# Kernel optimization log

Measured on AMD Instinct MI355X. Metric: run time of the kernel, lower is better.

The kernel has to match this reference:

```python
import jax, jax.numpy as jnp
import numpy as np


def setup_inputs() -> dict:
    key = jax.random.key(0)
    ks = jax.random.split(key, 5)
    b, n_q, n_kv = 16, 128, 4096
    query_dim, context_dim, heads, dim_head = 1024, 1024, 16, 64
    inner = heads * dim_head
    x = jax.random.normal(ks[0], (b, n_q, query_dim), dtype=jnp.float32)
    context = jax.random.normal(ks[1], (b, n_kv, context_dim), dtype=jnp.float32)
    # Linear weights stored as (in, out); scaled like default torch init magnitude
    Wq = jax.random.normal(ks[2], (query_dim, inner), dtype=jnp.float32) * (query_dim ** -0.5)
    Wkv = jax.random.normal(ks[3], (context_dim, 2 * inner), dtype=jnp.float32) * (context_dim ** -0.5)
    Wout = jax.random.normal(ks[4], (inner, query_dim), dtype=jnp.float32) * (inner ** -0.5)
    bout = jnp.zeros((query_dim,), dtype=jnp.float32)
    return {"x": x, "context": context, "Wq": Wq, "Wkv": Wkv, "Wout": Wout, "bout": bout}


def reference(x, context, Wq, Wkv, Wout, bout):
    heads, dim_head = 16, 64
    b, n_q, _ = x.shape
    n_kv = context.shape[1]
    scale = dim_head ** -0.5

    q = x @ Wq                       # [b, n_q, h*d]
    kv = context @ Wkv               # [b, n_kv, 2*h*d]
    k, v = jnp.split(kv, 2, axis=-1)

    def split_heads(t):
        bb, n, _ = t.shape
        return t.reshape(bb, n, heads, dim_head).transpose(0, 2, 1, 3)  # [b, h, n, d]

    q, k, v = map(split_heads, (q, k, v))

    # mask[i, j] = (i - (j % n_q) == 0)  -> query i attends keys j with j % n_q == i
    i_idx = jnp.arange(n_q)[:, None]
    j_idx = jnp.arange(n_kv)[None, :]
    mask = (j_idx % n_q) == i_idx      # [n_q, n_kv] bool

    sim = jnp.einsum('bhid,bhjd->bhij', q, k) * scale
    max_neg = -jnp.finfo(sim.dtype).max
    sim = jnp.where(mask[None, None, :, :], sim, max_neg)
    attn = jax.nn.softmax(sim, axis=-1)
    out = jnp.einsum('bhij,bhjd->bhid', attn, v)   # [b, h, n_q, d]
    out = out.transpose(0, 2, 1, 3).reshape(b, n_q, heads * dim_head)
    return out @ Wout + bout
```

## Files before the change

kernel.cpp:

```cpp
#include <hip/hip_runtime.h>
#include <hip/hip_bf16.h>

typedef __attribute__((ext_vector_type(8))) short short8;
typedef __attribute__((ext_vector_type(4))) float floatx4;

__device__ __forceinline__ unsigned short f32_to_bf16(float f) {
    unsigned int u = __builtin_bit_cast(unsigned int, f);
    u = (u + 0x7FFFu + ((u >> 16) & 1u)) >> 16;
    return (unsigned short)u;
}
__device__ __forceinline__ unsigned int pack_bf16x2(float lo, float hi) {
    return (unsigned int)f32_to_bf16(lo) | ((unsigned int)f32_to_bf16(hi) << 16);
}
__device__ __forceinline__ void async_load16(const unsigned short* g, unsigned short* l) {
    __builtin_amdgcn_global_load_lds(
        (const __attribute__((address_space(1))) void*)g,
        (__attribute__((address_space(3))) void*)l, 16, 0, 0);
}

__device__ __forceinline__ void transpose_tile(
    const float* __restrict__ W, int src_ld, int n_off,
    unsigned short* __restrict__ Wt, int dst_ld, int nb, int kb, int tid) {
    __shared__ float tile[32][33];
    int n0 = nb * 32, k0 = kb * 32;
    int tx = tid & 31, ty = tid >> 5;
#pragma unroll
    for (int p = 0; p < 4; ++p) {
        int r = ty + 8 * p;
        tile[r][tx] = W[(long)(k0 + r) * src_ld + n_off + n0 + tx];
    }
    __syncthreads();
#pragma unroll
    for (int p = 0; p < 4; ++p) {
        int r = ty + 8 * p;
        Wt[(long)(n0 + r) * dst_ld + k0 + tx] = f32_to_bf16(tile[tx][r]);
    }
}

__device__ __forceinline__ void cast8(
    const float* __restrict__ src, unsigned short* __restrict__ dst) {
    floatx4 a = *(const floatx4*)src;
    floatx4 b = *(const floatx4*)(src + 4);
    uint4 p;
    p.x = pack_bf16x2(a[0], a[1]); p.y = pack_bf16x2(a[2], a[3]);
    p.z = pack_bf16x2(b[0], b[1]); p.w = pack_bf16x2(b[2], b[3]);
    *(uint4*)dst = p;
}

__device__ __forceinline__ void cast8_nt(
    const float* __restrict__ src, unsigned short* __restrict__ dst) {
    floatx4 a = __builtin_nontemporal_load((const floatx4*)src);
    floatx4 b = __builtin_nontemporal_load((const floatx4*)(src + 4));
    uint4 p;
    p.x = pack_bf16x2(a[0], a[1]); p.y = pack_bf16x2(a[2], a[3]);
    p.z = pack_bf16x2(b[0], b[1]); p.w = pack_bf16x2(b[2], b[3]);
    *(uint4*)dst = p;
}

__global__ __launch_bounds__(256) void prep_kernel(
    const float* __restrict__ Wq, const float* __restrict__ Wkv,
    const float* __restrict__ Wout, const float* __restrict__ x,
    unsigned short* __restrict__ WqT, unsigned short* __restrict__ WkB,
    unsigned short* __restrict__ WvT, unsigned short* __restrict__ WoutT,
    unsigned short* __restrict__ xb) {
    int id = blockIdx.x, tid = threadIdx.x;
    if (id < 1024) { transpose_tile(Wq,   1024, 0,    WqT,   1024, id & 31, id >> 5, tid); return; }
    id -= 1024;
    if (id < 1024) { transpose_tile(Wkv,  2048, 1024, WvT,   1024, id & 31, id >> 5, tid); return; }
    id -= 1024;
    if (id < 1024) { transpose_tile(Wout, 1024, 0,    WoutT, 1024, id & 31, id >> 5, tid); return; }
    id -= 1024;
    if (id < 512) {
        long e = ((long)id * 256 + tid) * 8;
        long row = e >> 10, col = e & 1023;
        cast8(Wkv + row * 2048 + col, WkB + e);
        return;
    }
    id -= 512;
    { long e = ((long)id * 256 + tid) * 8; cast8(x + e, xb + e); }
}

__global__ __launch_bounds__(256, 4) void gemm64_kernel(
    const unsigned short* __restrict__ A, long sA, int lda,
    const unsigned short* __restrict__ Bt, long sB, int ldb,
    void* __restrict__ C, long sC, int ldc,
    const float* __restrict__ bias, int K, int out_bf16) {
    __shared__ unsigned short As[128 * 64];
    __shared__ unsigned short Bs[64 * 64];

    const int tid = threadIdx.x, wave = tid >> 6, lane = tid & 63;
    const int z = blockIdx.z;
    const int m0 = blockIdx.y * 128, n0 = blockIdx.x * 64;
    const unsigned short* Ab = A  + (long)z * sA + (long)m0 * lda;
    const unsigned short* Bb = Bt + (long)z * sB + (long)n0 * ldb;

    floatx4 acc[2][4];
#pragma unroll
    for (int i = 0; i < 2; ++i)
#pragma unroll
        for (int j = 0; j < 4; ++j) acc[i][j] = (floatx4)0.0f;

#pragma unroll
    for (int s = 0; s < 4; ++s) {
        int E = s * 2048 + tid * 8;
        int r = E >> 6, g = ((E >> 3) & 7) ^ (r & 7);
        async_load16(Ab + (long)r * lda + g * 8, &As[s * 2048 + wave * 512]);
    }
#pragma unroll
    for (int s = 0; s < 2; ++s) {
        int E = s * 2048 + tid * 8;
        int r = E >> 6, g = ((E >> 3) & 7) ^ (r & 7);
        async_load16(Bb + (long)r * ldb + g * 8, &Bs[s * 2048 + wave * 512]);
    }
    __syncthreads();

    const int frm = lane & 15, gq = lane >> 4;
    __builtin_amdgcn_s_setprio(1);
#pragma unroll
    for (int ks = 0; ks < 2; ++ks) {
        const int Ga = ks * 4 + gq;
        short8 a[2];
#pragma unroll
        for (int rt = 0; rt < 2; ++rt) {
            int Ra = wave * 32 + rt * 16 + frm;
            a[rt] = *(const short8*)&As[Ra * 64 + ((Ga ^ (Ra & 7)) << 3)];
        }
#pragma unroll
        for (int ct = 0; ct < 4; ++ct) {
            int Rb = ct * 16 + frm;
            short8 b = *(const short8*)&Bs[Rb * 64 + ((Ga ^ (Rb & 7)) << 3)];
#pragma unroll
            for (int rt = 0; rt < 2; ++rt)
                acc[rt][ct] = __builtin_amdgcn_mfma_f32_16x16x32_bf16(
                    a[rt], b, acc[rt][ct], 0, 0, 0);
        }
    }
    __builtin_amdgcn_s_setprio(0);

    const int orow0 = m0 + wave * 32 + (lane >> 4) * 4;
    const int ocol0 = n0 + (lane & 15);
    if (out_bf16) {
        unsigned short* Cb = (unsigned short*)C + (long)z * sC;
#pragma unroll
        for (int rt = 0; rt < 2; ++rt)
#pragma unroll
            for (int r = 0; r < 4; ++r) {
                long row = orow0 + rt * 16 + r;
#pragma unroll
                for (int ct = 0; ct < 4; ++ct)
                    Cb[row * ldc + ocol0 + ct * 16] = f32_to_bf16(acc[rt][ct][r]);
            }
    } else {
        float* Cf = (float*)C + (long)z * sC;
#pragma unroll
        for (int rt = 0; rt < 2; ++rt)
#pragma unroll
            for (int r = 0; r < 4; ++r) {
                long row = orow0 + rt * 16 + r;
#pragma unroll
                for (int ct = 0; ct < 4; ++ct) {
                    int col = ocol0 + ct * 16;
                    float v = acc[rt][ct][r];
                    if (bias) v += bias[col];
                    Cf[row * ldc + col] = v;
                }
            }
    }
}

__global__ __launch_bounds__(256, 4) void gemm64s_kernel(
    const unsigned short* __restrict__ A, long sA, int lda,
    const unsigned short* __restrict__ Bt, long sB, int ldb,
    void* __restrict__ C, long sC, int ldc,
    const float* __restrict__ bias, int K, int out_bf16) {
    __shared__ unsigned short As[2][64 * 64];
    __shared__ unsigned short Bs[2][64 * 64];

    const int tid = threadIdx.x, wave = tid >> 6, lane = tid & 63;
    const int z = blockIdx.z;
    const int m0 = blockIdx.y * 64, n0 = blockIdx.x * 64;
    const unsigned short* Ab = A  + (long)z * sA + (long)m0 * lda;
    const unsigned short* Bb = Bt + (long)z * sB + (long)n0 * ldb;

    floatx4 acc[4];
#pragma unroll
    for (int j = 0; j < 4; ++j) acc[j] = (floatx4)0.0f;

    const int frm = lane & 15, gq = lane >> 4;
    const int E0 = tid * 8;

    const int nt = K >> 6;
    int cur = 0;
#pragma unroll
    for (int s = 0; s < 2; ++s) {
        int E = s * 2048 + E0;
        int r = E >> 6, g = ((E >> 3) & 7) ^ (r & 7);
        async_load16(Ab + (long)r * lda + g * 8, &As[0][s * 2048 + wave * 512]);
        async_load16(Bb + (long)r * ldb + g * 8, &Bs[0][s * 2048 + wave * 512]);
    }

    for (int t = 0; t < nt; ++t) {
        __syncthreads();
        if (t + 1 < nt) {
            int kk = (t + 1) << 6;
#pragma unroll
            for (int s = 0; s < 2; ++s) {
                int E = s * 2048 + E0;
                int r = E >> 6, g = ((E >> 3) & 7) ^ (r & 7);
                async_load16(Ab + (long)r * lda + kk + g * 8,
                             &As[cur ^ 1][s * 2048 + wave * 512]);
                async_load16(Bb + (long)r * ldb + kk + g * 8,
                             &Bs[cur ^ 1][s * 2048 + wave * 512]);
            }
        }
        __builtin_amdgcn_s_setprio(1);
#pragma unroll
        for (int ks = 0; ks < 2; ++ks) {
            const int Ga = ks * 4 + gq;
            const int Ra = wave * 16 + frm;
            short8 a = *(const short8*)&As[cur][Ra * 64 + ((Ga ^ (Ra & 7)) << 3)];
#pragma unroll
            for (int ct = 0; ct < 4; ++ct) {
                int Rb = ct * 16 + frm;
                short8 b = *(const short8*)&Bs[cur][Rb * 64 + ((Ga ^ (Rb & 7)) << 3)];
                acc[ct] = __builtin_amdgcn_mfma_f32_16x16x32_bf16(
                    a, b, acc[ct], 0, 0, 0);
            }
        }
        __builtin_amdgcn_s_setprio(0);
        cur ^= 1;
    }

    const int orow0 = m0 + wave * 16 + (lane >> 4) * 4;
    const int ocol0 = n0 + (lane & 15);
    if (out_bf16) {
        unsigned short* Cb = (unsigned short*)C + (long)z * sC;
#pragma unroll
        for (int r = 0; r < 4; ++r) {
            long row = orow0 + r;
#pragma unroll
            for (int ct = 0; ct < 4; ++ct)
                Cb[row * ldc + ocol0 + ct * 16] = f32_to_bf16(acc[ct][r]);
        }
    } else {
        float* Cf = (float*)C + (long)z * sC;
#pragma unroll
        for (int r = 0; r < 4; ++r) {
            long row = orow0 + r;
#pragma unroll
            for (int ct = 0; ct < 4; ++ct) {
                int col = ocol0 + ct * 16;
                float v = acc[ct][r];
                if (bias) v += bias[col];
                Cf[row * ldc + col] = v;
            }
        }
    }
}

#define CLD 1032
__device__ __forceinline__ int swzb(int t, int c) {
    return t * (2 * CLD) + ((2 * c) ^ (((t >> 3) & 3) << 5));
}
__global__ __launch_bounds__(256, 2) void attn_fused_kernel(
    const float* __restrict__ ctx,
    const unsigned short* __restrict__ qt,
    unsigned short* __restrict__ wctx) {
    __shared__ unsigned short ctx_t[32 * CLD];
    __shared__ float sred[4 * 544];
    __shared__ unsigned short p_l[16 * 40];

    const int tid = threadIdx.x, wave = tid >> 6, lane = tid & 63;
    const int bi = blockIdx.x;
    const int b = bi >> 7, i = bi & 127;
    const int frm = lane & 15, fk = (lane >> 4) * 8;

    short8 af[8];
    const unsigned short* qbase =
        qt + (long)bi * 16384 + (long)frm * 1024 + wave * 256 + fk;
#pragma unroll
    for (int it = 0; it < 8; ++it) af[it] = *(const short8*)(qbase + it * 32);

#pragma unroll
    for (int rr = 0; rr < 16; ++rr) {
        int idx = rr * 2048 + tid * 8;
        int t = idx >> 10, c = idx & 1023;
        cast8_nt(ctx + ((long)b * 4096 + i + t * 128) * 1024 + c,
                 (unsigned short*)((char*)ctx_t + swzb(t, c)));
    }
    __syncthreads();

    floatx4 acc0 = (floatx4)0.0f, acc1 = (floatx4)0.0f;
    __builtin_amdgcn_s_setprio(1);
#pragma unroll
    for (int it = 0; it < 8; ++it) {
        int kk = wave * 256 + it * 32;
        short8 b0 = *(const short8*)((const char*)ctx_t + swzb(frm, kk + fk));
        short8 b1 = *(const short8*)((const char*)ctx_t + swzb(16 + frm, kk + fk));
        acc0 = __builtin_amdgcn_mfma_f32_16x16x32_bf16(af[it], b0, acc0, 0, 0, 0);
        acc1 = __builtin_amdgcn_mfma_f32_16x16x32_bf16(af[it], b1, acc1, 0, 0, 0);
    }
    __builtin_amdgcn_s_setprio(0);
#pragma unroll
    for (int r = 0; r < 4; ++r) {
        sred[wave * 544 + frm * 17 + (lane >> 4) * 4 + r]        = acc0[r];
        sred[wave * 544 + (16 + frm) * 17 + (lane >> 4) * 4 + r] = acc1[r];
    }
    __syncthreads();

    {
        const int h = wave * 4 + (lane >> 4);
        const int tg = lane & 15;
        const int i0 = tg * 17 + h, i1 = (16 + tg) * 17 + h;
        float s0 = (sred[i0] + sred[544 + i0] + sred[1088 + i0] + sred[1632 + i0]) * 0.125f;
        float s1 = (sred[i1] + sred[544 + i1] + sred[1088 + i1] + sred[1632 + i1]) * 0.125f;
        float m = fmaxf(s0, s1);
#pragma unroll
        for (int d = 1; d < 16; d <<= 1) m = fmaxf(m, __shfl_xor(m, d));
        float e0 = __expf(s0 - m), e1 = __expf(s1 - m);
        float den = e0 + e1;
#pragma unroll
        for (int d = 1; d < 16; d <<= 1) den += __shfl_xor(den, d);
        float inv = 1.0f / den;
        p_l[h * 40 + tg]      = f32_to_bf16(e0 * inv);
        p_l[h * 40 + 16 + tg] = f32_to_bf16(e1 * inv);
    }
    __syncthreads();

    short8 ap;
#pragma unroll
    for (int j = 0; j < 8; ++j) ap[j] = (short)p_l[frm * 40 + fk + j];

    unsigned short* wbase =
        wctx + (long)bi * 16384 + (long)frm * 1024 + (lane >> 4) * 4;
    __builtin_amdgcn_s_setprio(1);
#pragma unroll 4
    for (int nt = 0; nt < 16; ++nt) {
        int c0 = wave * 256 + nt * 16;
        short8 av;
#pragma unroll
        for (int j = 0; j < 8; ++j)
            av[j] = (short)*(const unsigned short*)
                        ((const char*)ctx_t + swzb(fk + j, c0 + frm));
        floatx4 wacc = __builtin_amdgcn_mfma_f32_16x16x32_bf16(
            av, ap, (floatx4)0.0f, 0, 0, 0);
        uint2 st;
        st.x = pack_bf16x2(wacc[0], wacc[1]);
        st.y = pack_bf16x2(wacc[2], wacc[3]);
        *(uint2*)(wbase + c0) = st;
    }
    __builtin_amdgcn_s_setprio(0);
}

extern "C" void kernel_launch(void* const* d_in, const int* in_sizes, int n_in,
                              void* d_out, int out_size, void* d_ws, size_t ws_size,
                              hipStream_t stream) {
    const float* x       = (const float*)d_in[0];
    const float* context = (const float*)d_in[1];
    const float* Wq      = (const float*)d_in[2];
    const float* Wkv     = (const float*)d_in[3];
    const float* Wout    = (const float*)d_in[4];
    const float* bout    = (const float*)d_in[5];
    float* out = (float*)d_out;

    char* ws = (char*)d_ws;
    unsigned short* WqT   = (unsigned short*)(ws);
    unsigned short* WkB   = (unsigned short*)(ws + (2ll  << 20));
    unsigned short* WvT   = (unsigned short*)(ws + (4ll  << 20));
    unsigned short* WoutT = (unsigned short*)(ws + (6ll  << 20));
    unsigned short* xb    = (unsigned short*)(ws + (8ll  << 20));
    unsigned short* qb    = (unsigned short*)(ws + (12ll << 20));
    unsigned short* aob   = (unsigned short*)(ws + (16ll << 20));
    unsigned short* qtb   = (unsigned short*)(ws + (32ll << 20));
    unsigned short* wctxb = (unsigned short*)(ws + (96ll << 20));

    prep_kernel<<<4608, 256, 0, stream>>>(Wq, Wkv, Wout, x, WqT, WkB, WvT, WoutT, xb);

    gemm64s_kernel<<<dim3(16, 32, 1), 256, 0, stream>>>(
        xb, 0, 1024, WqT, 0, 1024, qb, 0, 1024, nullptr, 1024, 1);
    gemm64_kernel<<<dim3(16, 16, 16), 256, 0, stream>>>(
        qb, 64, 1024, WkB, 64, 1024, qtb, 1024, 16384, nullptr, 64, 1);
    attn_fused_kernel<<<2048, 256, 0, stream>>>(context, qtb, wctxb);
    gemm64s_kernel<<<dim3(1, 32, 16), 256, 0, stream>>>(
        wctxb, 1024, 16384, WvT, (long)64 * 1024, 1024, aob, 64, 1024, nullptr, 1024, 1);
    gemm64s_kernel<<<dim3(16, 32, 1), 256, 0, stream>>>(
        aob, 0, 1024, WoutT, 0, 1024, out, 0, 1024, bout, 1024, 0);
}
```

Baseline: 446.9 us.

## Deepen GEMM async-load pipeline to 4 buffers and vectorize epilogue stores

The 64x64 GEMM now uses four LDS stages, prefetching two tiles ahead. It replaces the per-iteration __syncthreads with an explicit vmcnt wait plus s_barrier, so global-to-LDS latency is hidden better. Both GEMM kernels swap the MFMA operand order so each lane holds four consecutive output columns, which turns the scalar epilogue stores into 8- and 16-byte vector stores. The larger LDS footprint lowers the occupancy hint from 4 to 2 blocks per CU. The single barrier per iteration with a 4-deep ring is meant to keep overwritten buffers safe, but that relies on the vmcnt counting being exact.

```diff
diff --git a/kernel.cpp b/kernel.cpp
--- a/kernel.cpp
+++ b/kernel.cpp
@@ -3,6 +3,8 @@
 
 typedef __attribute__((ext_vector_type(8))) short short8;
 typedef __attribute__((ext_vector_type(4))) float floatx4;
+
+#define WAITV(N) asm volatile("s_waitcnt vmcnt(" #N ")" ::: "memory")
 
 __device__ __forceinline__ unsigned short f32_to_bf16(float f) {
     unsigned int u = __builtin_bit_cast(unsigned int, f);
@@ -132,49 +134,51 @@
 #pragma unroll
             for (int rt = 0; rt < 2; ++rt)
                 acc[rt][ct] = __builtin_amdgcn_mfma_f32_16x16x32_bf16(
-                    a[rt], b, acc[rt][ct], 0, 0, 0);
+                    b, a[rt], acc[rt][ct], 0, 0, 0);
         }
     }
     __builtin_amdgcn_s_setprio(0);
 
-    const int orow0 = m0 + wave * 32 + (lane >> 4) * 4;
-    const int ocol0 = n0 + (lane & 15);
+    const int oc0 = n0 + gq * 4;
     if (out_bf16) {
         unsigned short* Cb = (unsigned short*)C + (long)z * sC;
 #pragma unroll
-        for (int rt = 0; rt < 2; ++rt)
-#pragma unroll
-            for (int r = 0; r < 4; ++r) {
-                long row = orow0 + rt * 16 + r;
-#pragma unroll
-                for (int ct = 0; ct < 4; ++ct)
-                    Cb[row * ldc + ocol0 + ct * 16] = f32_to_bf16(acc[rt][ct][r]);
+        for (int rt = 0; rt < 2; ++rt) {
+            long row = m0 + wave * 32 + rt * 16 + frm;
+#pragma unroll
+            for (int ct = 0; ct < 4; ++ct) {
+                uint2 st;
+                st.x = pack_bf16x2(acc[rt][ct][0], acc[rt][ct][1]);
+                st.y = pack_bf16x2(acc[rt][ct][2], acc[rt][ct][3]);
+                *(uint2*)&Cb[row * ldc + oc0 + ct * 16] = st;
             }
+        }
     } else {
         float* Cf = (float*)C + (long)z * sC;
 #pragma unroll
-        for (int rt = 0; rt < 2; ++rt)
-#pragma unroll
-            for (int r = 0; r < 4; ++r) {
-                long row = orow0 + rt * 16 + r;
-#pragma unroll
-                for (int ct = 0; ct < 4; ++ct) {
-                    int col = ocol0 + ct * 16;
-                    float v = acc[rt][ct][r];
-                    if (bias) v += bias[col];
-                    Cf[row * ldc + col] = v;
+        for (int rt = 0; rt < 2; ++rt) {
+            long row = m0 + wave * 32 + rt * 16 + frm;
+#pragma unroll
+            for (int ct = 0; ct < 4; ++ct) {
+                int col = oc0 + ct * 16;
+                floatx4 v = acc[rt][ct];
+                if (bias) {
+#pragma unroll
+                    for (int j = 0; j < 4; ++j) v[j] += bias[col + j];
                 }
+                *(floatx4*)&Cf[row * ldc + col] = v;
             }
-    }
-}
-
-__global__ __launch_bounds__(256, 4) void gemm64s_kernel(
+        }
+    }
+}
+
+__global__ __launch_bounds__(256, 2) void gemm64s_kernel(
     const unsigned short* __restrict__ A, long sA, int lda,
     const unsigned short* __restrict__ Bt, long sB, int ldb,
     void* __restrict__ C, long sC, int ldc,
     const float* __restrict__ bias, int K, int out_bf16) {
-    __shared__ unsigned short As[2][64 * 64];
-    __shared__ unsigned short Bs[2][64 * 64];
+    __shared__ unsigned short As[4][64 * 64];
+    __shared__ unsigned short Bs[4][64 * 64];
 
     const int tid = threadIdx.x, wave = tid >> 6, lane = tid & 63;
     const int z = blockIdx.z;
@@ -188,72 +192,71 @@
 
     const int frm = lane & 15, gq = lane >> 4;
     const int E0 = tid * 8;
+    const int r0 = E0 >> 6,          g0 = ((E0 >> 3) & 7) ^ (r0 & 7);
+    const int r1 = (2048 + E0) >> 6, g1 = (((2048 + E0) >> 3) & 7) ^ (r1 & 7);
+
+#define STAGE(T, BUF) do {                                                    \
+        long kk_ = (long)(T) << 6;                                            \
+        async_load16(Ab + (long)r0 * lda + kk_ + g0 * 8, &As[BUF][wave * 512]);        \
+        async_load16(Ab + (long)r1 * lda + kk_ + g1 * 8, &As[BUF][2048 + wave * 512]); \
+        async_load16(Bb + (long)r0 * ldb + kk_ + g0 * 8, &Bs[BUF][wave * 512]);        \
+        async_load16(Bb + (long)r1 * ldb + kk_ + g1 * 8, &Bs[BUF][2048 + wave * 512]); \
+    } while (0)
 
     const int nt = K >> 6;
-    int cur = 0;
-#pragma unroll
-    for (int s = 0; s < 2; ++s) {
-        int E = s * 2048 + E0;
-        int r = E >> 6, g = ((E >> 3) & 7) ^ (r & 7);
-        async_load16(Ab + (long)r * lda + g * 8, &As[0][s * 2048 + wave * 512]);
-        async_load16(Bb + (long)r * ldb + g * 8, &Bs[0][s * 2048 + wave * 512]);
-    }
+    STAGE(0, 0);
+    if (nt > 1) STAGE(1, 1);
 
     for (int t = 0; t < nt; ++t) {
-        __syncthreads();
-        if (t + 1 < nt) {
-            int kk = (t + 1) << 6;
-#pragma unroll
-            for (int s = 0; s < 2; ++s) {
-                int E = s * 2048 + E0;
-                int r = E >> 6, g = ((E >> 3) & 7) ^ (r & 7);
-                async_load16(Ab + (long)r * lda + kk + g * 8,
-                             &As[cur ^ 1][s * 2048 + wave * 512]);
-                async_load16(Bb + (long)r * ldb + kk + g * 8,
-                             &Bs[cur ^ 1][s * 2048 + wave * 512]);
-            }
-        }
+        if (t + 2 < nt) { STAGE(t + 2, (t + 2) & 3); WAITV(8); }
+        else if (t + 1 < nt) { WAITV(4); }
+        else { WAITV(0); }
+        __builtin_amdgcn_sched_barrier(0);
+        __builtin_amdgcn_s_barrier();
+        __builtin_amdgcn_sched_barrier(0);
+
+        const unsigned short* as_ = As[t & 3];
+        const unsigned short* bs_ = Bs[t & 3];
         __builtin_amdgcn_s_setprio(1);
 #pragma unroll
         for (int ks = 0; ks < 2; ++ks) {
             const int Ga = ks * 4 + gq;
             const int Ra = wave * 16 + frm;
-            short8 a = *(const short8*)&As[cur][Ra * 64 + ((Ga ^ (Ra & 7)) << 3)];
+            short8 a = *(const short8*)&as_[Ra * 64 + ((Ga ^ (Ra & 7)) << 3)];
 #pragma unroll
             for (int ct = 0; ct < 4; ++ct) {
                 int Rb = ct * 16 + frm;
-                short8 b = *(const short8*)&Bs[cur][Rb * 64 + ((Ga ^ (Rb & 7)) << 3)];
+                short8 b = *(const short8*)&bs_[Rb * 64 + ((Ga ^ (Rb & 7)) << 3)];
                 acc[ct] = __builtin_amdgcn_mfma_f32_16x16x32_bf16(
-                    a, b, acc[ct], 0, 0, 0);
+                    b, a, acc[ct], 0, 0, 0);
             }
         }
         __builtin_amdgcn_s_setprio(0);
-        cur ^= 1;
-    }
-
-    const int orow0 = m0 + wave * 16 + (lane >> 4) * 4;
-    const int ocol0 = n0 + (lane & 15);
+    }
+#undef STAGE
+
+    const long orow = m0 + wave * 16 + frm;
+    const int oc0 = n0 + gq * 4;
     if (out_bf16) {
         unsigned short* Cb = (unsigned short*)C + (long)z * sC;
 #pragma unroll
-        for (int r = 0; r < 4; ++r) {
-            long row = orow0 + r;
-#pragma unroll
-            for (int ct = 0; ct < 4; ++ct)
-                Cb[row * ldc + ocol0 + ct * 16] = f32_to_bf16(acc[ct][r]);
+        for (int ct = 0; ct < 4; ++ct) {
+            uint2 st;
+            st.x = pack_bf16x2(acc[ct][0], acc[ct][1]);
+            st.y = pack_bf16x2(acc[ct][2], acc[ct][3]);
+            *(uint2*)&Cb[orow * ldc + oc0 + ct * 16] = st;
         }
     } else {
         float* Cf = (float*)C + (long)z * sC;
 #pragma unroll
-        for (int r = 0; r < 4; ++r) {
-            long row = orow0 + r;
-#pragma unroll
-            for (int ct = 0; ct < 4; ++ct) {
-                int col = ocol0 + ct * 16;
-                float v = acc[ct][r];
-                if (bias) v += bias[col];
-                Cf[row * ldc + col] = v;
+        for (int ct = 0; ct < 4; ++ct) {
+            int col = oc0 + ct * 16;
+            floatx4 v = acc[ct];
+            if (bias) {
+#pragma unroll
+                for (int j = 0; j < 4; ++j) v[j] += bias[col + j];
             }
+            *(floatx4*)&Cf[orow * ldc + col] = v;
         }
     }
 }
```

After: 450.2 us. About the same (+0.7%).
